# Optimization experiments

Hardware: AMD Instinct MI355X
Metric: run time of the kernel (lower is better)

The kernel has to match this reference:

```python
import jax, jax.numpy as jnp
import numpy as np

EPS_IN = 1e-5   # InstanceNorm2d default eps
EPS_VAR = 1e-6  # clamp on attention variance

def instance_norm(x):
    # x: (b, c, h, w); affine=False, biased variance over spatial dims
    mean = jnp.mean(x, axis=(2, 3), keepdims=True)
    var = jnp.var(x, axis=(2, 3), keepdims=True)
    return (x - mean) * jax.lax.rsqrt(var + EPS_IN)

def setup_inputs() -> dict:
    key = jax.random.key(0)
    k1, k2, k3, k4 = jax.random.split(key, 4)
    shp = (4, 512, 64, 64)
    return {
        "c_x": jax.random.normal(k1, shp, dtype=jnp.float32),
        "s_x": jax.random.normal(k2, shp, dtype=jnp.float32),
        "c_1x": jax.random.normal(k3, shp, dtype=jnp.float32),
        "s_1x": jax.random.normal(k4, shp, dtype=jnp.float32),
    }

def reference(c_x, s_x, c_1x, s_1x):
    b, v_dim, h, w = c_x.shape
    hw = h * w
    # Q: (b, hw, qk), K: (b, qk, hw), V: (b, hw, v)
    Q = instance_norm(c_1x).reshape(b, -1, hw).transpose(0, 2, 1)
    K = instance_norm(s_1x).reshape(b, -1, s_1x.shape[2] * s_1x.shape[3])
    V = s_x.reshape(b, v_dim, -1).transpose(0, 2, 1)
    # attention over spatial tokens
    A = jax.nn.softmax(jnp.einsum('bqc,bck->bqk', Q, K), axis=-1)
    M = jnp.einsum('bqk,bkv->bqv', A, V)              # weighted mean
    Var = jnp.einsum('bqk,bkv->bqv', A, V * V) - M * M  # weighted variance
    S = jnp.sqrt(jnp.clip(Var, EPS_VAR, None))
    # back to (b, v, h, w)
    M = M.reshape(b, h, w, -1).transpose(0, 3, 1, 2)
    S = S.reshape(b, h, w, -1).transpose(0, 3, 1, 2)
    return S * instance_norm(c_x) + M
```

## Files before the change

### kernel.cpp

```cpp
#include <hip/hip_runtime.h>
#include <cmath>


#define B_  4
#define C_  512
#define HW_ 4096

typedef _Float16 f16;
typedef _Float16 f16x8 __attribute__((ext_vector_type(8)));
typedef float    f32x4 __attribute__((ext_vector_type(4)));

__device__ __forceinline__ f32x4 mfma16(f16x8 a, f16x8 b, f32x4 c) {
  return __builtin_amdgcn_mfma_f32_16x16x32_f16(a, b, c, 0, 0, 0);
}
__device__ __forceinline__ void g2l16(const f16* g, f16* l) {
  __builtin_amdgcn_global_load_lds(
      (const __attribute__((address_space(1))) void*)g,
      (__attribute__((address_space(3))) void*)l, 16, 0, 0);
}

__global__ __launch_bounds__(256) void k_stats(
    const float* __restrict__ cx, const float* __restrict__ c1,
    const float* __restrict__ s1,
    float2* __restrict__ cxs, float2* __restrict__ c1s, float2* __restrict__ s1s) {
  int c = blockIdx.x, b = blockIdx.y, t = blockIdx.z;
  const float* src = (t == 0 ? cx : (t == 1 ? c1 : s1)) + (size_t)(b * C_ + c) * HW_;
  float s = 0.f, q = 0.f;
  const float4* src4 = (const float4*)src;
  for (int i = threadIdx.x; i < HW_ / 4; i += 256) {
    float4 v = src4[i];
    s += v.x + v.y + v.z + v.w;
    q += v.x * v.x + v.y * v.y + v.z * v.z + v.w * v.w;
  }
#pragma unroll
  for (int off = 1; off < 64; off <<= 1) {
    s += __shfl_xor(s, off);
    q += __shfl_xor(q, off);
  }
  __shared__ float ss[4], sq[4];
  int wv = threadIdx.x >> 6;
  if ((threadIdx.x & 63) == 0) { ss[wv] = s; sq[wv] = q; }
  __syncthreads();
  if (threadIdx.x == 0) {
    float S = ss[0] + ss[1] + ss[2] + ss[3];
    float Q = sq[0] + sq[1] + sq[2] + sq[3];
    float mean = S * (1.f / HW_);
    float var = Q * (1.f / HW_) - mean * mean;
    float2 r;
    r.x = mean;
    r.y = rsqrtf(var + 1e-5f);
    (t == 0 ? cxs : (t == 1 ? c1s : s1s))[b * C_ + c] = r;
  }
}

__global__ __launch_bounds__(256) void k_prept(
    const float* __restrict__ src, const float2* __restrict__ st,
    f16* __restrict__ dst) {
  int pb = blockIdx.x * 64, cb = blockIdx.y * 64, b = blockIdx.z;
  __shared__ float t[64][65];
  int tj = threadIdx.x & 63, tr = threadIdx.x >> 6;
#pragma unroll 4
  for (int p = 0; p < 16; ++p) {
    int cl = p * 4 + tr;
    float2 mr = st[b * C_ + cb + cl];
    float v = src[(size_t)(b * C_ + cb + cl) * HW_ + pb + tj];
    t[cl][tj] = (v - mr.x) * mr.y;
  }
  __syncthreads();
#pragma unroll 4
  for (int p = 0; p < 16; ++p) {
    int pr = p * 4 + tr;
    dst[(size_t)(b * HW_ + pb + pr) * C_ + cb + tj] = (f16)t[tj][pr];
  }
}

__global__ __launch_bounds__(256) void k_prepv(const float* __restrict__ src,
                                               f16* __restrict__ vcat) {
  int gid = blockIdx.x * 256 + threadIdx.x;
  int bc = gid >> 9;
  int ko = (gid & 511) * 8;
  const float4* s = (const float4*)(src + (size_t)bc * HW_ + ko);
  float4 v0 = s[0], v1 = s[1];
  f16x8 v = {(f16)v0.x, (f16)v0.y, (f16)v0.z, (f16)v0.w,
             (f16)v1.x, (f16)v1.y, (f16)v1.z, (f16)v1.w};
  f16x8 v2 = v * v;
  int b = bc >> 9, c = bc & 511;
  f16* d = vcat + ((size_t)(b * 1024 + 2 * c)) * HW_ + ko;
  *(f16x8*)d = v;
  *(f16x8*)(d + HW_) = v2;
}

__global__ __launch_bounds__(256, 2) void k_qk(
    const f16* __restrict__ Qt, const f16* __restrict__ Kt,
    f16* __restrict__ E, float2* __restrict__ mlpart,
    int qspan, int qt128, int npair) {
  int id = blockIdx.x, pair, kt;
  if ((npair & 7) == 0) {
    int xcd = id & 7, j = id >> 3, qrs = npair >> 3;
    pair = xcd * qrs + (j % qrs);
    kt = j / qrs;
  } else {
    pair = id >> 4;
    kt = id & 15;
  }
  int bz = pair / qt128, qt = pair - bz * qt128;

  const f16* Aq = Qt + ((size_t)(bz * qspan + qt * 128)) * C_;
  const f16* Bk = Kt + (size_t)bz * HW_ * C_ + (size_t)kt * 256 * C_;
  f16* Eb = E + ((size_t)(bz * qspan + qt * 128)) * HW_ + kt * 256;
  float2* mlb = mlpart + ((size_t)(bz * qspan + qt * 128)) * 16 + kt;

  __shared__ __align__(16) f16 As[128 * 32], Bs[256 * 32];
  __shared__ float sred[2][128];

  int t = threadIdx.x, wave = t >> 6, lane = t & 63, lq = lane & 15, quad = lane >> 4;
  int wy = wave >> 1, wx = wave & 1;
  int srow = t >> 2, scol = (t & 3) * 8;

  f32x4 acc[4][8];
#pragma unroll
  for (int mt = 0; mt < 4; ++mt)
#pragma unroll
    for (int nt = 0; nt < 8; ++nt) acc[mt][nt] = (f32x4){0, 0, 0, 0};

  for (int kc = 0; kc < 16; ++kc) {
    __syncthreads();
    g2l16(Aq + (size_t)srow * C_ + kc * 32 + scol, As + t * 8);
    g2l16(Aq + (size_t)(srow + 64) * C_ + kc * 32 + scol, As + 2048 + t * 8);
#pragma unroll
    for (int i = 0; i < 4; ++i)
      g2l16(Bk + (size_t)(srow + 64 * i) * C_ + kc * 32 + scol,
            Bs + i * 2048 + t * 8);
    __syncthreads();
    f16x8 af[4], bf[8];
#pragma unroll
    for (int mt = 0; mt < 4; ++mt)
      af[mt] = *(const f16x8*)(As + (wy * 64 + mt * 16 + lq) * 32 + quad * 8);
#pragma unroll
    for (int nt = 0; nt < 8; ++nt)
      bf[nt] = *(const f16x8*)(Bs + (wx * 128 + nt * 16 + lq) * 32 + quad * 8);
#pragma unroll
    for (int mt = 0; mt < 4; ++mt)
#pragma unroll
      for (int nt = 0; nt < 8; ++nt)
        acc[mt][nt] = mfma16(af[mt], bf[nt], acc[mt][nt]);
  }

#pragma unroll
  for (int mt = 0; mt < 4; ++mt)
#pragma unroll
    for (int r = 0; r < 4; ++r) {
      float v = -1e30f;
#pragma unroll
      for (int nt = 0; nt < 8; ++nt) v = fmaxf(v, acc[mt][nt][r]);
#pragma unroll
      for (int msk = 1; msk < 16; msk <<= 1) v = fmaxf(v, __shfl_xor(v, msk));
      if (lq == 0) sred[wx][wy * 64 + mt * 16 + quad * 4 + r] = v;
    }
  __syncthreads();
  float mrow[4][4];
#pragma unroll
  for (int mt = 0; mt < 4; ++mt)
#pragma unroll
    for (int r = 0; r < 4; ++r) {
      int rr = wy * 64 + mt * 16 + quad * 4 + r;
      mrow[mt][r] = fmaxf(sred[0][rr], sred[1][rr]);
    }
  __syncthreads();

  float rsum[4][4];
#pragma unroll
  for (int mt = 0; mt < 4; ++mt)
#pragma unroll
    for (int r = 0; r < 4; ++r) rsum[mt][r] = 0.f;
#pragma unroll
  for (int mt = 0; mt < 4; ++mt)
#pragma unroll
    for (int nt = 0; nt < 8; ++nt) {
      f32x4 v = acc[mt][nt];
#pragma unroll
      for (int r = 0; r < 4; ++r) {
        float e = __expf(v[r] - mrow[mt][r]);
        rsum[mt][r] += e;
        Eb[(size_t)(wy * 64 + mt * 16 + quad * 4 + r) * HW_ +
           wx * 128 + nt * 16 + lq] = (f16)e;
      }
    }
#pragma unroll
  for (int mt = 0; mt < 4; ++mt)
#pragma unroll
    for (int r = 0; r < 4; ++r) {
      float v = rsum[mt][r];
#pragma unroll
      for (int msk = 1; msk < 16; msk <<= 1) v += __shfl_xor(v, msk);
      if (lq == 0) sred[wx][wy * 64 + mt * 16 + quad * 4 + r] = v;
    }
  __syncthreads();
  if (wx == 0 && lq == 0) {
#pragma unroll
    for (int mt = 0; mt < 4; ++mt)
#pragma unroll
      for (int r = 0; r < 4; ++r) {
        int rr = wy * 64 + mt * 16 + quad * 4 + r;
        mlb[(size_t)rr * 16] = make_float2(mrow[mt][r], sred[0][rr] + sred[1][rr]);
      }
  }
}

__global__ __launch_bounds__(256) void k_red(const float2* __restrict__ mlpart,
                                             float* __restrict__ alpha) {
  int row = blockIdx.x * 256 + threadIdx.x;
  const float2* p = mlpart + (size_t)row * 16;
  float2 loc[16];
  float m = -1e30f;
#pragma unroll
  for (int i = 0; i < 16; ++i) {
    loc[i] = p[i];
    m = fmaxf(m, loc[i].x);
  }
  float l = 0.f;
#pragma unroll
  for (int i = 0; i < 16; ++i) l += loc[i].y * __expf(loc[i].x - m);
  float invl = 1.f / l;
#pragma unroll
  for (int i = 0; i < 16; ++i)
    alpha[(size_t)row * 16 + i] = __expf(loc[i].x - m) * invl;
}

__global__ __launch_bounds__(256, 2) void k_pv(
    const f16* __restrict__ P, const float* __restrict__ alphaG,
    const f16* __restrict__ Vcat, const float* __restrict__ cx,
    const float2* __restrict__ cxs, float* __restrict__ out,
    int qspan, int qbase, int qt128) {
  int npairs = (int)gridDim.x >> 2;
  int id = blockIdx.x, pair, ct;
  if ((npairs & 7) == 0) {
    int x = id & 7, j = id >> 3, ppx = npairs >> 3;
    pair = x * ppx + (j >> 2);
    ct = j & 3;
  } else {
    pair = id >> 2;
    ct = id & 3;
  }
  int bz = pair / qt128, qt = pair - bz * qt128;

  const f16* Ap = P + ((size_t)(bz * qspan + qt * 128)) * HW_;
  const f16* Bv = Vcat + ((size_t)(bz * 1024 + ct * 256)) * HW_;

  __shared__ __align__(16) f16 As[128 * 32], Bs[256 * 32];
  __shared__ float Al[128 * 17];

  int t = threadIdx.x, wave = t >> 6, lane = t & 63, lq = lane & 15, quad = lane >> 4;
  int wy = wave >> 1, wx = wave & 1;
  int srow = t >> 2, scol = (t & 3) * 8;

  {
    const float* ag = alphaG + ((size_t)(bz * qspan + qt * 128)) * 16;
#pragma unroll
    for (int i = 0; i < 8; ++i) {
      int e = i * 256 + t;
      Al[(e >> 4) * 17 + (e & 15)] = ag[e];
    }
  }

  f32x4 acc[4][8];
#pragma unroll
  for (int mt = 0; mt < 4; ++mt)
#pragma unroll
    for (int nt = 0; nt < 8; ++nt) acc[mt][nt] = (f32x4){0, 0, 0, 0};

  for (int kc = 0; kc < 128; ++kc) {
    __syncthreads();
    g2l16(Ap + (size_t)srow * HW_ + kc * 32 + scol, As + t * 8);
    g2l16(Ap + (size_t)(srow + 64) * HW_ + kc * 32 + scol, As + 2048 + t * 8);
#pragma unroll
    for (int i = 0; i < 4; ++i)
      g2l16(Bv + (size_t)(srow + 64 * i) * HW_ + kc * 32 + scol,
            Bs + i * 2048 + t * 8);
    __syncthreads();

    int ktl = kc >> 3;
    f16x8 af[4];
    f16x8 bf[8];
#pragma unroll
    for (int mt = 0; mt < 4; ++mt) {
      af[mt] = *(const f16x8*)(As + (wy * 64 + mt * 16 + lq) * 32 + quad * 8);
      f16 a = (f16)Al[(wy * 64 + mt * 16 + lq) * 17 + ktl];
      af[mt] = af[mt] * a;
    }
#pragma unroll
    for (int nt = 0; nt < 8; ++nt)
      bf[nt] = *(const f16x8*)(Bs + (wx * 128 + nt * 16 + lq) * 32 + quad * 8);
#pragma unroll
    for (int mt = 0; mt < 4; ++mt)
#pragma unroll
      for (int nt = 0; nt < 8; ++nt)
        acc[mt][nt] = mfma16(af[mt], bf[nt], acc[mt][nt]);
  }

  int ch2base = ct * 256 + wx * 128;
#pragma unroll
  for (int mt = 0; mt < 4; ++mt) {
    int q0 = qbase + qt * 128 + wy * 64 + mt * 16 + quad * 4;
#pragma unroll
    for (int nt = 0; nt < 8; ++nt) {
      f32x4 m1 = acc[mt][nt];
      f32x4 m2;
#pragma unroll
      for (int r = 0; r < 4; ++r) m2[r] = __shfl_xor(m1[r], 1);
      if (!(lane & 1)) {
        int c = (ch2base + nt * 16 + lq) >> 1;
        float2 st = cxs[bz * C_ + c];
        size_t base = ((size_t)bz * C_ + c) * HW_ + q0;
        float4 cv = *(const float4*)(cx + base);
        float4 o;
        o.x = sqrtf(fmaxf(m2[0] - m1[0] * m1[0], 1e-6f)) * ((cv.x - st.x) * st.y) + m1[0];
        o.y = sqrtf(fmaxf(m2[1] - m1[1] * m1[1], 1e-6f)) * ((cv.y - st.x) * st.y) + m1[1];
        o.z = sqrtf(fmaxf(m2[2] - m1[2] * m1[2], 1e-6f)) * ((cv.z - st.x) * st.y) + m1[2];
        o.w = sqrtf(fmaxf(m2[3] - m1[3] * m1[3], 1e-6f)) * ((cv.w - st.x) * st.y) + m1[3];
        *(float4*)(out + base) = o;
      }
    }
  }
}

extern "C" void kernel_launch(void* const* d_in, const int* in_sizes, int n_in,
                              void* d_out, int out_size, void* d_ws,
                              size_t ws_size, hipStream_t stream) {
  const float* c_x = (const float*)d_in[0];
  const float* s_x = (const float*)d_in[1];
  const float* c1x = (const float*)d_in[2];
  const float* s1x = (const float*)d_in[3];
  float* out = (float*)d_out;

  char* ws = (char*)d_ws;
  size_t o = 0;
  f16* Qt = (f16*)(ws + o);  o += (size_t)B_ * HW_ * C_ * 2;
  f16* Kt = (f16*)(ws + o);  o += (size_t)B_ * HW_ * C_ * 2;
  f16* Vcat = (f16*)(ws + o); o += (size_t)B_ * HW_ * 1024 * 2;
  float2* cxs = (float2*)(ws + o); o += B_ * C_ * sizeof(float2);
  float2* c1s = (float2*)(ws + o); o += B_ * C_ * sizeof(float2);
  float2* s1s = (float2*)(ws + o); o += B_ * C_ * sizeof(float2);
  size_t fixed = (o + 255) & ~(size_t)255;

  const size_t per_row = (size_t)HW_ * 2 + 16 * 8 + 16 * 4;
  struct Cfg { int nb, qs; };
  const Cfg cfgs[5] = {{4, 4096}, {1, 4096}, {1, 2048}, {1, 1024}, {1, 512}};
  Cfg cfg = cfgs[4];
  for (int i = 0; i < 5; ++i) {
    size_t rows = (size_t)cfgs[i].nb * cfgs[i].qs;
    if (fixed + rows * per_row <= ws_size) { cfg = cfgs[i]; break; }
  }
  const int nb = cfg.nb, qspan = cfg.qs, qt128 = qspan / 128;
  const int npair = nb * qt128;
  const size_t rows = (size_t)nb * qspan;
  f16* E = (f16*)(ws + fixed);
  float2* mlpart = (float2*)(ws + fixed + rows * HW_ * 2);
  float* alpha = (float*)(ws + fixed + rows * HW_ * 2 + rows * 16 * 8);

  k_stats<<<dim3(C_, B_, 3), 256, 0, stream>>>(c_x, c1x, s1x, cxs, c1s, s1s);
  k_prept<<<dim3(HW_ / 64, C_ / 64, B_), 256, 0, stream>>>(c1x, c1s, Qt);
  k_prept<<<dim3(HW_ / 64, C_ / 64, B_), 256, 0, stream>>>(s1x, s1s, Kt);
  k_prepv<<<dim3(B_ * C_ * HW_ / 8 / 256), 256, 0, stream>>>(s_x, Vcat);

  for (int b0 = 0; b0 < B_; b0 += nb) {
    for (int qb = 0; qb < HW_; qb += qspan) {
      const f16* Qtp = Qt + ((size_t)b0 * HW_ + qb) * C_;
      const f16* Ktp = Kt + (size_t)b0 * HW_ * C_;
      const f16* Vcp = Vcat + (size_t)b0 * 1024 * HW_;
      const float* cxp = c_x + (size_t)b0 * C_ * HW_;
      const float2* cxsp = cxs + b0 * C_;
      float* outp = out + (size_t)b0 * C_ * HW_;

      k_qk<<<dim3((unsigned)(npair * 16)), 256, 0, stream>>>(
          Qtp, Ktp, E, mlpart, qspan, qt128, npair);
      k_red<<<dim3((unsigned)(rows / 256)), 256, 0, stream>>>(mlpart, alpha);
      k_pv<<<dim3((unsigned)(npair * 4)), 256, 0, stream>>>(
          E, alpha, Vcp, cxp, cxsp, outp, qspan, qb, qt128);
    }
  }
}
```

Before: 465.8 us.

## Compute V squared in registers and stage softmax E stores through LDS

The PV kernel now loads only fp16 V and squares the fragments in registers, keeping separate accumulators for mean and second moment. This replaces the precomputed interleaved V/V² buffer, halving B-operand traffic and prep writes. The QK kernel writes exponentiated scores into a shared-memory tile (aliased with the operand buffers) and then stores them with 16-byte coalesced writes instead of scattered 2-byte stores. This costs extra barriers and some VALU work per k-step.

New measurement: 423.9 us. -9.0%, faster.

```diff
diff --git a/kernel.cpp b/kernel.cpp
--- a/kernel.cpp
+++ b/kernel.cpp
@@ -75,19 +75,13 @@
 }
 
 __global__ __launch_bounds__(256) void k_prepv(const float* __restrict__ src,
-                                               f16* __restrict__ vcat) {
+                                               f16* __restrict__ dst) {
   int gid = blockIdx.x * 256 + threadIdx.x;
-  int bc = gid >> 9;
-  int ko = (gid & 511) * 8;
-  const float4* s = (const float4*)(src + (size_t)bc * HW_ + ko);
+  const float4* s = (const float4*)src + (size_t)gid * 2;
   float4 v0 = s[0], v1 = s[1];
   f16x8 v = {(f16)v0.x, (f16)v0.y, (f16)v0.z, (f16)v0.w,
              (f16)v1.x, (f16)v1.y, (f16)v1.z, (f16)v1.w};
-  f16x8 v2 = v * v;
-  int b = bc >> 9, c = bc & 511;
-  f16* d = vcat + ((size_t)(b * 1024 + 2 * c)) * HW_ + ko;
-  *(f16x8*)d = v;
-  *(f16x8*)(d + HW_) = v2;
+  *(f16x8*)(dst + (size_t)gid * 8) = v;
 }
 
 __global__ __launch_bounds__(256, 2) void k_qk(
@@ -110,8 +104,13 @@
   f16* Eb = E + ((size_t)(bz * qspan + qt * 128)) * HW_ + kt * 256;
   float2* mlb = mlpart + ((size_t)(bz * qspan + qt * 128)) * 16 + kt;
 
-  __shared__ __align__(16) f16 As[128 * 32], Bs[256 * 32];
+  __shared__ __align__(16) union ShQK {
+    struct { f16 As[128 * 32]; f16 Bs[256 * 32]; } s;
+    f16 ebuf[32 * 272];
+  } sh;
   __shared__ float sred[2][128];
+  f16* As = sh.s.As;
+  f16* Bs = sh.s.Bs;
 
   int t = threadIdx.x, wave = t >> 6, lane = t & 63, lq = lane & 15, quad = lane >> 4;
   int wy = wave >> 1, wx = wave & 1;
@@ -166,15 +165,16 @@
       int rr = wy * 64 + mt * 16 + quad * 4 + r;
       mrow[mt][r] = fmaxf(sred[0][rr], sred[1][rr]);
     }
-  __syncthreads();
 
   float rsum[4][4];
 #pragma unroll
   for (int mt = 0; mt < 4; ++mt)
 #pragma unroll
     for (int r = 0; r < 4; ++r) rsum[mt][r] = 0.f;
-#pragma unroll
-  for (int mt = 0; mt < 4; ++mt)
+
+#pragma unroll
+  for (int mt = 0; mt < 4; ++mt) {
+    __syncthreads();
 #pragma unroll
     for (int nt = 0; nt < 8; ++nt) {
       f32x4 v = acc[mt][nt];
@@ -182,10 +182,20 @@
       for (int r = 0; r < 4; ++r) {
         float e = __expf(v[r] - mrow[mt][r]);
         rsum[mt][r] += e;
-        Eb[(size_t)(wy * 64 + mt * 16 + quad * 4 + r) * HW_ +
-           wx * 128 + nt * 16 + lq] = (f16)e;
+        sh.ebuf[(wy * 16 + quad * 4 + r) * 272 + wx * 128 + nt * 16 + lq] = (f16)e;
       }
     }
+    __syncthreads();
+#pragma unroll
+    for (int i = 0; i < 4; ++i) {
+      int idx = i * 256 + t;
+      int rl = idx >> 5, cs = (idx & 31) * 8;
+      f16x8 v8 = *(const f16x8*)(sh.ebuf + rl * 272 + cs);
+      int grow = (rl >> 4) * 64 + mt * 16 + (rl & 15);
+      *(f16x8*)(Eb + (size_t)grow * HW_ + cs) = v8;
+    }
+  }
+
 #pragma unroll
   for (int mt = 0; mt < 4; ++mt)
 #pragma unroll
@@ -229,7 +239,7 @@
 
 __global__ __launch_bounds__(256, 2) void k_pv(
     const f16* __restrict__ P, const float* __restrict__ alphaG,
-    const f16* __restrict__ Vcat, const float* __restrict__ cx,
+    const f16* __restrict__ V, const float* __restrict__ cx,
     const float2* __restrict__ cxs, float* __restrict__ out,
     int qspan, int qbase, int qt128) {
   int npairs = (int)gridDim.x >> 2;
@@ -245,9 +255,9 @@
   int bz = pair / qt128, qt = pair - bz * qt128;
 
   const f16* Ap = P + ((size_t)(bz * qspan + qt * 128)) * HW_;
-  const f16* Bv = Vcat + ((size_t)(bz * 1024 + ct * 256)) * HW_;
-
-  __shared__ __align__(16) f16 As[128 * 32], Bs[256 * 32];
+  const f16* Bv = V + ((size_t)(bz * C_ + ct * 128)) * HW_;
+
+  __shared__ __align__(16) f16 As[128 * 32], Bs[128 * 32];
   __shared__ float Al[128 * 17];
 
   int t = threadIdx.x, wave = t >> 6, lane = t & 63, lq = lane & 15, quad = lane >> 4;
@@ -263,25 +273,25 @@
     }
   }
 
-  f32x4 acc[4][8];
-#pragma unroll
-  for (int mt = 0; mt < 4; ++mt)
-#pragma unroll
-    for (int nt = 0; nt < 8; ++nt) acc[mt][nt] = (f32x4){0, 0, 0, 0};
+  f32x4 accM[4][4], accM2[4][4];
+#pragma unroll
+  for (int mt = 0; mt < 4; ++mt)
+#pragma unroll
+    for (int nt = 0; nt < 4; ++nt) {
+      accM[mt][nt] = (f32x4){0, 0, 0, 0};
+      accM2[mt][nt] = (f32x4){0, 0, 0, 0};
+    }
 
   for (int kc = 0; kc < 128; ++kc) {
     __syncthreads();
     g2l16(Ap + (size_t)srow * HW_ + kc * 32 + scol, As + t * 8);
     g2l16(Ap + (size_t)(srow + 64) * HW_ + kc * 32 + scol, As + 2048 + t * 8);
-#pragma unroll
-    for (int i = 0; i < 4; ++i)
-      g2l16(Bv + (size_t)(srow + 64 * i) * HW_ + kc * 32 + scol,
-            Bs + i * 2048 + t * 8);
+    g2l16(Bv + (size_t)srow * HW_ + kc * 32 + scol, Bs + t * 8);
+    g2l16(Bv + (size_t)(srow + 64) * HW_ + kc * 32 + scol, Bs + 2048 + t * 8);
     __syncthreads();
 
     int ktl = kc >> 3;
-    f16x8 af[4];
-    f16x8 bf[8];
+    f16x8 af[4], bf[4], bf2[4];
 #pragma unroll
     for (int mt = 0; mt < 4; ++mt) {
       af[mt] = *(const f16x8*)(As + (wy * 64 + mt * 16 + lq) * 32 + quad * 8);
@@ -289,37 +299,36 @@
       af[mt] = af[mt] * a;
     }
 #pragma unroll
-    for (int nt = 0; nt < 8; ++nt)
-      bf[nt] = *(const f16x8*)(Bs + (wx * 128 + nt * 16 + lq) * 32 + quad * 8);
+    for (int nt = 0; nt < 4; ++nt) {
+      bf[nt] = *(const f16x8*)(Bs + (wx * 64 + nt * 16 + lq) * 32 + quad * 8);
+      bf2[nt] = bf[nt] * bf[nt];
+    }
 #pragma unroll
     for (int mt = 0; mt < 4; ++mt)
 #pragma unroll
-      for (int nt = 0; nt < 8; ++nt)
-        acc[mt][nt] = mfma16(af[mt], bf[nt], acc[mt][nt]);
-  }
-
-  int ch2base = ct * 256 + wx * 128;
+      for (int nt = 0; nt < 4; ++nt) {
+        accM[mt][nt] = mfma16(af[mt], bf[nt], accM[mt][nt]);
+        accM2[mt][nt] = mfma16(af[mt], bf2[nt], accM2[mt][nt]);
+      }
+  }
+
+  int chbase = ct * 128 + wx * 64;
 #pragma unroll
   for (int mt = 0; mt < 4; ++mt) {
     int q0 = qbase + qt * 128 + wy * 64 + mt * 16 + quad * 4;
 #pragma unroll
-    for (int nt = 0; nt < 8; ++nt) {
-      f32x4 m1 = acc[mt][nt];
-      f32x4 m2;
-#pragma unroll
-      for (int r = 0; r < 4; ++r) m2[r] = __shfl_xor(m1[r], 1);
-      if (!(lane & 1)) {
-        int c = (ch2base + nt * 16 + lq) >> 1;
-        float2 st = cxs[bz * C_ + c];
-        size_t base = ((size_t)bz * C_ + c) * HW_ + q0;
-        float4 cv = *(const float4*)(cx + base);
-        float4 o;
-        o.x = sqrtf(fmaxf(m2[0] - m1[0] * m1[0], 1e-6f)) * ((cv.x - st.x) * st.y) + m1[0];
-        o.y = sqrtf(fmaxf(m2[1] - m1[1] * m1[1], 1e-6f)) * ((cv.y - st.x) * st.y) + m1[1];
-        o.z = sqrtf(fmaxf(m2[2] - m1[2] * m1[2], 1e-6f)) * ((cv.z - st.x) * st.y) + m1[2];
-        o.w = sqrtf(fmaxf(m2[3] - m1[3] * m1[3], 1e-6f)) * ((cv.w - st.x) * st.y) + m1[3];
-        *(float4*)(out + base) = o;
-      }
+    for (int nt = 0; nt < 4; ++nt) {
+      int c = chbase + nt * 16 + lq;
+      float2 st = cxs[bz * C_ + c];
+      size_t base = ((size_t)bz * C_ + c) * HW_ + q0;
+      float4 cv = *(const float4*)(cx + base);
+      f32x4 m1 = accM[mt][nt], m2 = accM2[mt][nt];
+      float4 o;
+      o.x = sqrtf(fmaxf(m2[0] - m1[0] * m1[0], 1e-6f)) * ((cv.x - st.x) * st.y) + m1[0];
+      o.y = sqrtf(fmaxf(m2[1] - m1[1] * m1[1], 1e-6f)) * ((cv.y - st.x) * st.y) + m1[1];
+      o.z = sqrtf(fmaxf(m2[2] - m1[2] * m1[2], 1e-6f)) * ((cv.z - st.x) * st.y) + m1[2];
+      o.w = sqrtf(fmaxf(m2[3] - m1[3] * m1[3], 1e-6f)) * ((cv.w - st.x) * st.y) + m1[3];
+      *(float4*)(out + base) = o;
     }
   }
 }
@@ -337,7 +346,7 @@
   size_t o = 0;
   f16* Qt = (f16*)(ws + o);  o += (size_t)B_ * HW_ * C_ * 2;
   f16* Kt = (f16*)(ws + o);  o += (size_t)B_ * HW_ * C_ * 2;
-  f16* Vcat = (f16*)(ws + o); o += (size_t)B_ * HW_ * 1024 * 2;
+  f16* Vh = (f16*)(ws + o);  o += (size_t)B_ * HW_ * C_ * 2;
   float2* cxs = (float2*)(ws + o); o += B_ * C_ * sizeof(float2);
   float2* c1s = (float2*)(ws + o); o += B_ * C_ * sizeof(float2);
   float2* s1s = (float2*)(ws + o); o += B_ * C_ * sizeof(float2);
@@ -361,13 +370,13 @@
   k_stats<<<dim3(C_, B_, 3), 256, 0, stream>>>(c_x, c1x, s1x, cxs, c1s, s1s);
   k_prept<<<dim3(HW_ / 64, C_ / 64, B_), 256, 0, stream>>>(c1x, c1s, Qt);
   k_prept<<<dim3(HW_ / 64, C_ / 64, B_), 256, 0, stream>>>(s1x, s1s, Kt);
-  k_prepv<<<dim3(B_ * C_ * HW_ / 8 / 256), 256, 0, stream>>>(s_x, Vcat);
+  k_prepv<<<dim3(B_ * C_ * HW_ / 8 / 256), 256, 0, stream>>>(s_x, Vh);
 
   for (int b0 = 0; b0 < B_; b0 += nb) {
     for (int qb = 0; qb < HW_; qb += qspan) {
       const f16* Qtp = Qt + ((size_t)b0 * HW_ + qb) * C_;
       const f16* Ktp = Kt + (size_t)b0 * HW_ * C_;
-      const f16* Vcp = Vcat + (size_t)b0 * 1024 * HW_;
+      const f16* Vp = Vh + (size_t)b0 * C_ * HW_;
       const float* cxp = c_x + (size_t)b0 * C_ * HW_;
       const float2* cxsp = cxs + b0 * C_;
       float* outp = out + (size_t)b0 * C_ * HW_;
@@ -376,7 +385,7 @@
           Qtp, Ktp, E, mlpart, qspan, qt128, npair);
       k_red<<<dim3((unsigned)(rows / 256)), 256, 0, stream>>>(mlpart, alpha);
       k_pv<<<dim3((unsigned)(npair * 4)), 256, 0, stream>>>(
-          E, alpha, Vcp, cxp, cxsp, outp, qspan, qb, qt128);
-    }
-  }
-}
+          E, alpha, Vp, cxp, cxsp, outp, qspan, qb, qt128);
+    }
+  }
+}
```
